# Kernel optimization log

Hardware: AMD Instinct MI355X
Metric: run time of the kernel (lower is better)

## Reference

```python
import jax, jax.numpy as jnp
import numpy as np

NUM_CLUSTERS = 16
CHANNELS = 256
UPDATE_RATE = 0.2
# channels % num_clusters == 0 -> all cluster capacities equal
_BASE = CHANNELS // NUM_CLUSTERS
_REM = CHANNELS % NUM_CLUSTERS
CLUSTER_SIZES = jnp.asarray([_BASE + 1] * _REM + [_BASE] * (NUM_CLUSTERS - _REM), dtype=jnp.int32)


def _cdist(a, b):
    # euclidean pairwise distance, batched over leading dims
    d2 = (jnp.sum(a * a, -1)[..., :, None]
          + jnp.sum(b * b, -1)[..., None, :]
          - 2.0 * (a @ jnp.swapaxes(b, -1, -2)))
    return jnp.sqrt(jnp.clip(d2, 0.0))


def _fps(D, k):
    # farthest point sampling given full [N,N] distance matrix
    start = jnp.argmax(D.sum(1))
    def step(min_d, _):
        far = jnp.argmax(min_d)
        return jnp.minimum(min_d, D[far]), far
    _, rest = jax.lax.scan(step, D[start], None, length=k - 1)
    return jnp.concatenate([start[None], rest])


def _capacity_assign(D, sizes):
    # greedy fixed-capacity assignment, sequential over channels
    order = jnp.argsort(D, axis=1)  # [C, K] cluster preference per channel
    def step(counts, row):
        avail = counts[row] < sizes[row]
        chosen = row[jnp.argmax(avail)]  # first available preference
        return counts.at[chosen].add(1), chosen
    _, assign = jax.lax.scan(step, jnp.zeros(sizes.shape[0], jnp.int32), order)
    return assign


def setup_inputs() -> dict:
    key = jax.random.key(0)
    k1, k2 = jax.random.split(key)
    features = jax.random.normal(k1, (8, CHANNELS, 64, 256), dtype=jnp.float32)
    pos_emb_batch = jax.random.normal(k2, (8, CHANNELS, 3), dtype=jnp.float32)
    return {"features": features, "pos_emb_batch": pos_emb_batch}


def reference(features, pos_emb_batch):
    b, c, nw, df = features.shape
    K = NUM_CLUSTERS
    pos = pos_emb_batch[0]                                   # [C, 3] (module's pos_emb buffer)
    # _initialize_centers: FPS over electrode positions
    centers = pos[_fps(_cdist(pos, pos), K)]                 # [K, 3]
    # _find_farthest_channels (euclidean): FPS over flattened features per batch
    ff = features.reshape(b, c, -1)
    Db = _cdist(ff, ff)                                      # [b, C, C]
    sel = jax.vmap(lambda D: _fps(D, K))(Db)                 # [b, K]
    # _cluster_euclidean_temp: nearest temp center per channel
    center_coords = pos_emb_batch[jnp.arange(b)[:, None], sel]      # [b, K, 3]
    temp_assign = jnp.argmin(_cdist(pos_emb_batch, center_coords), -1)  # [b, C]
    # per-cluster mean of positions over the whole batch
    flat_a = temp_assign.reshape(-1)
    flat_p = pos_emb_batch.reshape(-1, 3)
    sums = jax.ops.segment_sum(flat_p, flat_a, num_segments=K)
    cnts = jax.ops.segment_sum(jnp.ones(flat_a.shape, jnp.float32), flat_a, num_segments=K)
    avg = jnp.where(cnts[:, None] > 0, sums / jnp.maximum(cnts, 1.0)[:, None], 0.0)
    # match old centers to batch-average temp centers and EMA update
    matching = jnp.argmin(_cdist(centers, avg), axis=1)
    centers = (1.0 - UPDATE_RATE) * centers + UPDATE_RATE * avg[matching]
    # capacity-constrained final assignment
    return _capacity_assign(_cdist(pos, centers), CLUSTER_SIZES)
```

## Files before the change

### kernel.cpp

```cpp
#include <hip/hip_runtime.h>
#include <hip/hip_cooperative_groups.h>

namespace cg = cooperative_groups;

#define NB 8
#define NC 256
#define DF 16384
#define KCL 16
#define SPLITS 16
#define KC (DF / SPLITS)
#define BK 32
#define ITERS (KC / BK)
#define NPAIR 3
#define GEMM_BLOCKS (NPAIR * 2 * NB * SPLITS)

typedef _Float16 half8 __attribute__((ext_vector_type(8)));
typedef _Float16 half4_t __attribute__((ext_vector_type(4)));
typedef float floatx4 __attribute__((ext_vector_type(4)));

__device__ const int TItab[NPAIR] = {0,0,1};
__device__ const int TJtab[NPAIR] = {0,1,1};

__device__ __forceinline__ int argmax256w(float v, float* sv, int* si) {
  int t = threadIdx.x;
  float bv = v; int bi = t;
  #pragma unroll
  for (int s = 32; s >= 1; s >>= 1) {
    float ov = __shfl_down(bv, s);
    int   oi = __shfl_down(bi, s);
    if (ov > bv || (ov == bv && oi < bi)) { bv = ov; bi = oi; }
  }
  int w = t >> 6;
  if ((t & 63) == 0) { sv[w] = bv; si[w] = bi; }
  __syncthreads();
  float rbv = sv[0]; int rbi = si[0];
  #pragma unroll
  for (int k = 1; k < 4; ++k) {
    float ov = sv[k]; int oi = si[k];
    if (ov > rbv || (ov == rbv && oi < rbi)) { rbv = ov; rbi = oi; }
  }
  __syncthreads();
  return rbi;
}

__device__ __forceinline__ int argmax512p(float v, float* sv, int* si) {
  int t = threadIdx.x;
  sv[t] = v; si[t] = t;
  __syncthreads();
  #pragma unroll
  for (int s = 256; s >= 1; s >>= 1) {
    if (t < s) {
      float a = sv[t], b = sv[t + s];
      int ia = si[t], ib = si[t + s];
      if (b > a || (b == a && ib < ia)) { sv[t] = b; si[t] = ib; }
    }
    __syncthreads();
  }
  int r = si[0];
  __syncthreads();
  return r;
}

__global__ __launch_bounds__(512, 3) void k_gemm_pre(const float* __restrict__ ff,
                                                     const float* __restrict__ pe,
                                                     float* __restrict__ Pp,
                                                     float* __restrict__ centers0,
                                                     float* __restrict__ rs) {
  __shared__ _Float16 Ah[128][40];
  __shared__ _Float16 Al[128][40];
  __shared__ _Float16 Bh[64][40];
  __shared__ _Float16 Bl[64][40];

  const int bid = blockIdx.x;
  const int tid = threadIdx.x;

  if (bid == GEMM_BLOCKS) {
    float* sm = (float*)&Ah[0][0];
    float* px = sm;        float* py = sm + 256;
    float* pz = sm + 512;  float* pn = sm + 768;
    float* sv = sm + 1024; int*   si = (int*)(sm + 1536);
    int* fpsIdx = (int*)(sm + 2048);
    const int t = tid;
    for (int i = t; i < NB * NC; i += 512) rs[i] = 0.f;
    const bool valid = t < NC;
    float x = 0.f, y = 0.f, z = 0.f, n = 0.f;
    if (valid) {
      x = pe[t * 3 + 0]; y = pe[t * 3 + 1]; z = pe[t * 3 + 2];
      n = x * x + y * y + z * z;
      px[t] = x; py[t] = y; pz[t] = z; pn[t] = n;
    }
    __syncthreads();
    float rsum = -3.4e38f;
    if (valid) {
      rsum = 0.f;
      for (int j = 0; j < NC; ++j) {
        float dot = x * px[j] + y * py[j] + z * pz[j];
        rsum += sqrtf(fmaxf(n + pn[j] - 2.f * dot, 0.f));
      }
    }
    int start = argmax512p(rsum, sv, si);
    if (t == 0) fpsIdx[0] = start;
    float mind = -3.4e38f;
    if (valid) {
      float dot0 = x * px[start] + y * py[start] + z * pz[start];
      mind = sqrtf(fmaxf(n + pn[start] - 2.f * dot0, 0.f));
    }
    for (int it = 1; it < KCL; ++it) {
      int far = argmax512p(mind, sv, si);
      if (t == 0) fpsIdx[it] = far;
      if (valid) {
        float dot = x * px[far] + y * py[far] + z * pz[far];
        mind = fminf(mind, sqrtf(fmaxf(n + pn[far] - 2.f * dot, 0.f)));
      }
    }
    __syncthreads();
    if (t < KCL) {
      int p = fpsIdx[t];
      centers0[t * 3 + 0] = px[p];
      centers0[t * 3 + 1] = py[p];
      centers0[t * 3 + 2] = pz[p];
    }
    return;
  }

  const int x    = bid & 7;
  const int slot = bid >> 3;
  const int tc   = slot % 6;
  const int u    = slot / 6;
  const int gi   = x * 16 + u;
  const int b    = gi & 7;
  const int sp   = gi >> 3;

  const int pair = tc >> 1, ch = tc & 1;
  const int ti = TItab[pair], tj = TJtab[pair];
  const bool diag = (ti == tj);

  const int wave = tid >> 6, lane = tid & 63;
  const int wr = wave >> 1, wc = wave & 1;
  const int lrow = lane & 15, q = lane >> 4;

  const int srA = tid >> 2, scA = (tid & 3) * 8;
  const int srB = tid >> 3, scB = (tid & 7) * 4;
  const float* gA = ff + ((size_t)(b * NC + ti * 128 + srA)) * DF + sp * KC + scA;
  const float* gB = ff + ((size_t)(b * NC + tj * 128 + ch * 64 + srB)) * DF + sp * KC + scB;

  floatx4 a1[2][2], a2[2][2], a3[2][2];
  #pragma unroll
  for (int i = 0; i < 2; ++i)
    #pragma unroll
    for (int j = 0; j < 2; ++j) { a1[i][j] = (floatx4)0.f; a2[i][j] = (floatx4)0.f; a3[i][j] = (floatx4)0.f; }

  float4 ra0 = *(const float4*)(gA), ra1 = *(const float4*)(gA + 4);
  float4 rb = make_float4(0.f, 0.f, 0.f, 0.f);
  if (!diag) rb = *(const float4*)(gB);
  gA += BK; gB += BK;

  for (int it = 0; it < ITERS; ++it) {
    float fa[8] = {ra0.x, ra0.y, ra0.z, ra0.w, ra1.x, ra1.y, ra1.z, ra1.w};
    half8 ah, al;
    #pragma unroll
    for (int e = 0; e < 8; ++e) {
      _Float16 h = (_Float16)fa[e];
      ah[e] = h;
      al[e] = (_Float16)(fa[e] - (float)h);
    }
    half4_t bh4 = (half4_t)(_Float16)0.f, bl4 = (half4_t)(_Float16)0.f;
    if (!diag) {
      float fb[4] = {rb.x, rb.y, rb.z, rb.w};
      #pragma unroll
      for (int e = 0; e < 4; ++e) {
        _Float16 h = (_Float16)fb[e];
        bh4[e] = h;
        bl4[e] = (_Float16)(fb[e] - (float)h);
      }
    }
    __syncthreads();
    *(half8*)&Ah[srA][scA] = ah;
    *(half8*)&Al[srA][scA] = al;
    if (!diag) {
      *(half4_t*)&Bh[srB][scB] = bh4;
      *(half4_t*)&Bl[srB][scB] = bl4;
    }
    __syncthreads();
    if (it + 1 < ITERS) {
      ra0 = *(const float4*)(gA); ra1 = *(const float4*)(gA + 4);
      if (!diag) rb = *(const float4*)(gB);
      gA += BK; gB += BK;
    }
    const _Float16* bhp = diag ? &Ah[ch * 64][0] : &Bh[0][0];
    const _Float16* blp = diag ? &Al[ch * 64][0] : &Bl[0][0];
    half8 af[2], lf[2];
    #pragma unroll
    for (int i = 0; i < 2; ++i) {
      af[i] = *(const half8*)&Ah[wr * 32 + i * 16 + lrow][q * 8];
      lf[i] = *(const half8*)&Al[wr * 32 + i * 16 + lrow][q * 8];
    }
    #pragma unroll
    for (int j = 0; j < 2; ++j) {
      half8 bhf = *(const half8*)(bhp + (wc * 32 + j * 16 + lrow) * 40 + q * 8);
      half8 blf = *(const half8*)(blp + (wc * 32 + j * 16 + lrow) * 40 + q * 8);
      #pragma unroll
      for (int i = 0; i < 2; ++i) {
        a1[i][j] = __builtin_amdgcn_mfma_f32_16x16x32_f16(af[i], bhf, a1[i][j], 0, 0, 0);
        a2[i][j] = __builtin_amdgcn_mfma_f32_16x16x32_f16(af[i], blf, a2[i][j], 0, 0, 0);
        a3[i][j] = __builtin_amdgcn_mfma_f32_16x16x32_f16(lf[i], bhf, a3[i][j], 0, 0, 0);
      }
    }
  }

  float* Pb = Pp + (size_t)(sp * NB + b) * NC * NC;
  #pragma unroll
  for (int i = 0; i < 2; ++i) {
    int grow = ti * 128 + wr * 32 + i * 16 + q * 4;
    #pragma unroll
    for (int j = 0; j < 2; ++j) {
      int gcol = tj * 128 + ch * 64 + wc * 32 + j * 16 + lrow;
      float4 v;
      v.x = a1[i][j][0] + a2[i][j][0] + a3[i][j][0];
      v.y = a1[i][j][1] + a2[i][j][1] + a3[i][j][1];
      v.z = a1[i][j][2] + a2[i][j][2] + a3[i][j][2];
      v.w = a1[i][j][3] + a2[i][j][3] + a3[i][j][3];
      Pb[(size_t)(grow + 0) * NC + gcol] = v.x;
      Pb[(size_t)(grow + 1) * NC + gcol] = v.y;
      Pb[(size_t)(grow + 2) * NC + gcol] = v.z;
      Pb[(size_t)(grow + 3) * NC + gcol] = v.w;
      if (!diag) *(float4*)&Pb[(size_t)gcol * NC + grow] = v;
    }
  }
}

__global__ __launch_bounds__(256) void k_tail(const float* __restrict__ Pp,
                                              float* __restrict__ Db,
                                              float* __restrict__ rs,
                                              const float* __restrict__ pe,
                                              float* __restrict__ ccoord,
                                              const float* __restrict__ centers0,
                                              int* __restrict__ outp) {
  cg::grid_group grid = cg::this_grid();
  const int t = threadIdx.x;

  {
    __shared__ float dg_s[NC];
    const int b = blockIdx.x >> 5, i0 = (blockIdx.x & 31) * 8;
    float s = 0.f;
    #pragma unroll
    for (int sp = 0; sp < SPLITS; ++sp)
      s += Pp[((size_t)(sp * NB + b) * NC + t) * NC + t];
    dg_s[t] = s;
    __syncthreads();
    float colsum = 0.f;
    for (int ii = 0; ii < 8; ++ii) {
      int i = i0 + ii;
      float acc = 0.f;
      #pragma unroll
      for (int sp = 0; sp < SPLITS; ++sp)
        acc += Pp[((size_t)(sp * NB + b) * NC + i) * NC + t];
      float d2 = dg_s[i] + dg_s[t] - 2.f * acc;
      float d = sqrtf(fmaxf(d2, 0.f));
      Db[((size_t)b * NC + i) * NC + t] = d;
      colsum += d;
    }
    atomicAdd(&rs[b * NC + t], colsum);
  }
  grid.sync();

  {
    __shared__ float sv[4]; __shared__ int si[4];
    __shared__ int fpsIdx[KCL];
    if (blockIdx.x < NB) {
      int b = blockIdx.x;
      const float* D = Db + (size_t)b * NC * NC;
      int start = argmax256w(rs[b * NC + t], sv, si);
      if (t == 0) fpsIdx[0] = start;
      float mind = D[start * NC + t];
      for (int it = 1; it < KCL; ++it) {
        int far = argmax256w(mind, sv, si);
        if (t == 0) fpsIdx[it] = far;
        mind = fminf(mind, D[far * NC + t]);
      }
      __syncthreads();
      if (t < KCL) {
        int p = fpsIdx[t];
        ccoord[(b * KCL + t) * 3 + 0] = pe[(b * NC + p) * 3 + 0];
        ccoord[(b * KCL + t) * 3 + 1] = pe[(b * NC + p) * 3 + 1];
        ccoord[(b * KCL + t) * 3 + 2] = pe[(b * NC + p) * 3 + 2];
      }
    }
  }
  grid.sync();

  if (blockIdx.x == 0) {
    __shared__ float cc[NB * KCL * 3];
    __shared__ float cn[NB * KCL];
    __shared__ float sums[KCL][3];
    __shared__ int cnts[KCL];
    __shared__ float avg[KCL][3];
    __shared__ float an[KCL];
    __shared__ float c0[KCL * 3];
    __shared__ float c1x[KCL], c1y[KCL], c1z[KCL], c1n[KCL];
    __shared__ int order[NC][KCL];
    for (int i = t; i < NB * KCL * 3; i += 256) cc[i] = ccoord[i];
    if (t < KCL * 3) c0[t] = centers0[t];
    if (t < KCL) { sums[t][0] = 0.f; sums[t][1] = 0.f; sums[t][2] = 0.f; cnts[t] = 0; }
    __syncthreads();
    if (t < NB * KCL) {
      float x = cc[t * 3], y = cc[t * 3 + 1], z = cc[t * 3 + 2];
      cn[t] = x * x + y * y + z * z;
    }
    __syncthreads();
    for (int b = 0; b < NB; ++b) {
      int p = b * NC + t;
      float x = pe[p * 3], y = pe[p * 3 + 1], z = pe[p * 3 + 2];
      float n = x * x + y * y + z * z;
      float best = 3.4e38f; int bi = 0;
      #pragma unroll
      for (int k = 0; k < KCL; ++k) {
        int c = b * KCL + k;
        float dot = x * cc[c * 3] + y * cc[c * 3 + 1] + z * cc[c * 3 + 2];
        float d2 = fmaxf(n + cn[c] - 2.f * dot, 0.f);
        if (d2 < best) { best = d2; bi = k; }
      }
      atomicAdd(&sums[bi][0], x);
      atomicAdd(&sums[bi][1], y);
      atomicAdd(&sums[bi][2], z);
      atomicAdd(&cnts[bi], 1);
    }
    __syncthreads();
    if (t < KCL) {
      float c = (float)cnts[t];
      float inv = 1.f / fmaxf(c, 1.f);
      float ax = (cnts[t] > 0) ? sums[t][0] * inv : 0.f;
      float ay = (cnts[t] > 0) ? sums[t][1] * inv : 0.f;
      float az = (cnts[t] > 0) ? sums[t][2] * inv : 0.f;
      avg[t][0] = ax; avg[t][1] = ay; avg[t][2] = az;
      an[t] = ax * ax + ay * ay + az * az;
    }
    __syncthreads();
    if (t < KCL) {
      float x = c0[t * 3], y = c0[t * 3 + 1], z = c0[t * 3 + 2];
      float n = x * x + y * y + z * z;
      float best = 3.4e38f; int bi = 0;
      #pragma unroll
      for (int j = 0; j < KCL; ++j) {
        float dot = x * avg[j][0] + y * avg[j][1] + z * avg[j][2];
        float d2 = fmaxf(n + an[j] - 2.f * dot, 0.f);
        if (d2 < best) { best = d2; bi = j; }
      }
      float nx = 0.8f * x + 0.2f * avg[bi][0];
      float ny = 0.8f * y + 0.2f * avg[bi][1];
      float nz = 0.8f * z + 0.2f * avg[bi][2];
      c1x[t] = nx; c1y[t] = ny; c1z[t] = nz;
      c1n[t] = nx * nx + ny * ny + nz * nz;
    }
    __syncthreads();
    {
      float x = pe[t * 3], y = pe[t * 3 + 1], z = pe[t * 3 + 2];
      float n = x * x + y * y + z * z;
      float v[KCL];
      #pragma unroll
      for (int k = 0; k < KCL; ++k) {
        float dot = x * c1x[k] + y * c1y[k] + z * c1z[k];
        v[k] = fmaxf(n + c1n[k] - 2.f * dot, 0.f);
      }
      bool used[KCL];
      #pragma unroll
      for (int k = 0; k < KCL; ++k) used[k] = false;
      for (int r = 0; r < KCL; ++r) {
        float best = 3.4e38f; int bi = 0;
        #pragma unroll
        for (int j = 0; j < KCL; ++j) {
          if (!used[j] && v[j] < best) { best = v[j]; bi = j; }
        }
        order[t][r] = bi;
        used[bi] = true;
      }
    }
    __syncthreads();
    if (t < 64) {
      int cnt = 0;
      int cur = (t < KCL) ? order[0][t] : 0;
      for (int i = 0; i < NC; ++i) {
        int nxt = (t < KCL && i + 1 < NC) ? order[i + 1][t] : 0;
        int ccur = __shfl(cnt, cur);
        bool avail = (t < KCL) && (ccur < 16);
        unsigned long long m = __ballot(avail);
        int chosen;
        if (m != 0ull) {
          int rank = __ffsll((unsigned long long)m) - 1;
          chosen = __shfl(cur, rank);
        } else {
          chosen = __shfl(cur, 0);
        }
        if (t == chosen) cnt++;
        if (t == 0) outp[i] = chosen;
        cur = nxt;
      }
    }
  }
}

extern "C" void kernel_launch(void* const* d_in, const int* in_sizes, int n_in,
                              void* d_out, int out_size, void* d_ws, size_t ws_size,
                              hipStream_t stream) {
  (void)in_sizes; (void)n_in; (void)out_size; (void)ws_size;
  const float* features = (const float*)d_in[0];
  const float* pe = (const float*)d_in[1];
  char* ws = (char*)d_ws;
  float* Pp       = (float*)(ws);
  float* Db       = (float*)(ws + 33554432);
  float* rs       = (float*)(ws + 35651584);
  float* centers0 = (float*)(ws + 35659776);
  float* ccoord   = (float*)(ws + 35660288);
  int*   outp     = (int*)d_out;

  hipLaunchKernelGGL(k_gemm_pre, dim3(GEMM_BLOCKS + 1), dim3(512), 0, stream,
                     features, pe, Pp, centers0, rs);

  void* targs[] = {(void*)&Pp, (void*)&Db, (void*)&rs, (void*)&pe,
                   (void*)&ccoord, (void*)&centers0, (void*)&outp};
  hipLaunchCooperativeKernel((void*)k_tail, dim3(256), dim3(256), targs, 0, stream);
}
```

Baseline: 393.4 us.

## Replace cooperative tail kernel with separate launches and atomic-flag handoff

Splits the cooperative k_tail kernel (two grid.syncs) into k_formD (2048 blocks, one row each) and k_fps_final (8 blocks). The final clustering stage waits on an atomic counter in block 0 instead of a grid barrier. The GEMM now also writes the Gram diagonal into a small dgp buffer, so k_formD no longer gathers strided diagonal entries from the split partials. This removes cooperative-launch and grid-barrier overhead, at the cost of an extra kernel launch, one global atomic per element for the row sums, and a spin-wait that depends on all 8 blocks being resident.

After: 332.2 us. -15.6%, faster.

```diff
diff --git a/kernel.cpp b/kernel.cpp
--- a/kernel.cpp
+++ b/kernel.cpp
@@ -1,7 +1,4 @@
 #include <hip/hip_runtime.h>
-#include <hip/hip_cooperative_groups.h>
-
-namespace cg = cooperative_groups;
 
 #define NB 8
 #define NC 256
@@ -65,7 +62,8 @@
                                                      const float* __restrict__ pe,
                                                      float* __restrict__ Pp,
                                                      float* __restrict__ centers0,
-                                                     float* __restrict__ rs) {
+                                                     float* __restrict__ rs,
+                                                     float* __restrict__ dgp) {
   __shared__ _Float16 Ah[128][40];
   __shared__ _Float16 Al[128][40];
   __shared__ _Float16 Bh[64][40];
@@ -224,177 +222,189 @@
       Pb[(size_t)(grow + 1) * NC + gcol] = v.y;
       Pb[(size_t)(grow + 2) * NC + gcol] = v.z;
       Pb[(size_t)(grow + 3) * NC + gcol] = v.w;
-      if (!diag) *(float4*)&Pb[(size_t)gcol * NC + grow] = v;
-    }
-  }
-}
-
-__global__ __launch_bounds__(256) void k_tail(const float* __restrict__ Pp,
-                                              float* __restrict__ Db,
-                                              float* __restrict__ rs,
-                                              const float* __restrict__ pe,
-                                              float* __restrict__ ccoord,
-                                              const float* __restrict__ centers0,
-                                              int* __restrict__ outp) {
-  cg::grid_group grid = cg::this_grid();
+      if (!diag) {
+        *(float4*)&Pb[(size_t)gcol * NC + grow] = v;
+      } else {
+        int dr = gcol - grow;
+        if (dr >= 0 && dr < 4) {
+          float vr = (dr == 0) ? v.x : (dr == 1) ? v.y : (dr == 2) ? v.z : v.w;
+          dgp[(sp * NB + b) * NC + gcol] = vr;
+        }
+      }
+    }
+  }
+}
+
+__global__ __launch_bounds__(256) void k_formD(const float* __restrict__ Pp,
+                                               const float* __restrict__ dgp,
+                                               float* __restrict__ Db,
+                                               float* __restrict__ rs,
+                                               int* __restrict__ fps_done) {
   const int t = threadIdx.x;
-
+  const int b = blockIdx.x >> 8;
+  const int i = blockIdx.x & 255;
+  if (blockIdx.x == 0 && t == 0) *fps_done = 0;
+  float dgt = 0.f;
+  #pragma unroll
+  for (int sp = 0; sp < SPLITS; ++sp)
+    dgt += dgp[(sp * NB + b) * NC + t];
+  __shared__ float dgi_s;
+  if (t == i) dgi_s = dgt;
+  __syncthreads();
+  float dgi = dgi_s;
+  float acc = 0.f;
+  #pragma unroll
+  for (int sp = 0; sp < SPLITS; ++sp)
+    acc += Pp[((size_t)(sp * NB + b) * NC + i) * NC + t];
+  float d2 = dgi + dgt - 2.f * acc;
+  float d = sqrtf(fmaxf(d2, 0.f));
+  Db[((size_t)b * NC + i) * NC + t] = d;
+  atomicAdd(&rs[b * NC + t], d);
+}
+
+__global__ __launch_bounds__(256) void k_fps_final(const float* __restrict__ Db,
+                                                   const float* __restrict__ rs,
+                                                   const float* __restrict__ pe,
+                                                   const float* __restrict__ centers0,
+                                                   float* __restrict__ ccoord,
+                                                   int* __restrict__ fps_done,
+                                                   int* __restrict__ outp) {
+  const int b = blockIdx.x, t = threadIdx.x;
+  __shared__ float sv[4]; __shared__ int si[4];
+  __shared__ int fpsIdx[KCL];
   {
-    __shared__ float dg_s[NC];
-    const int b = blockIdx.x >> 5, i0 = (blockIdx.x & 31) * 8;
-    float s = 0.f;
-    #pragma unroll
-    for (int sp = 0; sp < SPLITS; ++sp)
-      s += Pp[((size_t)(sp * NB + b) * NC + t) * NC + t];
-    dg_s[t] = s;
-    __syncthreads();
-    float colsum = 0.f;
-    for (int ii = 0; ii < 8; ++ii) {
-      int i = i0 + ii;
-      float acc = 0.f;
-      #pragma unroll
-      for (int sp = 0; sp < SPLITS; ++sp)
-        acc += Pp[((size_t)(sp * NB + b) * NC + i) * NC + t];
-      float d2 = dg_s[i] + dg_s[t] - 2.f * acc;
-      float d = sqrtf(fmaxf(d2, 0.f));
-      Db[((size_t)b * NC + i) * NC + t] = d;
-      colsum += d;
-    }
-    atomicAdd(&rs[b * NC + t], colsum);
-  }
-  grid.sync();
-
+    const float* D = Db + (size_t)b * NC * NC;
+    int start = argmax256w(rs[b * NC + t], sv, si);
+    if (t == 0) fpsIdx[0] = start;
+    float mind = D[start * NC + t];
+    for (int it = 1; it < KCL; ++it) {
+      int far = argmax256w(mind, sv, si);
+      if (t == 0) fpsIdx[it] = far;
+      mind = fminf(mind, D[far * NC + t]);
+    }
+    __syncthreads();
+    if (t < KCL) {
+      int p = fpsIdx[t];
+      ccoord[(b * KCL + t) * 3 + 0] = pe[(b * NC + p) * 3 + 0];
+      ccoord[(b * KCL + t) * 3 + 1] = pe[(b * NC + p) * 3 + 1];
+      ccoord[(b * KCL + t) * 3 + 2] = pe[(b * NC + p) * 3 + 2];
+    }
+  }
+  __syncthreads();
+  if (t == 0)
+    __hip_atomic_fetch_add(fps_done, 1, __ATOMIC_RELEASE, __HIP_MEMORY_SCOPE_AGENT);
+  if (b != 0) return;
+
+  if (t == 0) {
+    while (__hip_atomic_load(fps_done, __ATOMIC_ACQUIRE, __HIP_MEMORY_SCOPE_AGENT) < NB)
+      __builtin_amdgcn_s_sleep(8);
+  }
+  __syncthreads();
+
+  __shared__ float cc[NB * KCL * 3];
+  __shared__ float cn[NB * KCL];
+  __shared__ float sums[KCL][3];
+  __shared__ int cnts[KCL];
+  __shared__ float avg[KCL][3];
+  __shared__ float an[KCL];
+  __shared__ float c0[KCL * 3];
+  __shared__ float c1x[KCL], c1y[KCL], c1z[KCL], c1n[KCL];
+  __shared__ int order[NC][KCL];
+  for (int i = t; i < NB * KCL * 3; i += 256) cc[i] = ccoord[i];
+  if (t < KCL * 3) c0[t] = centers0[t];
+  if (t < KCL) { sums[t][0] = 0.f; sums[t][1] = 0.f; sums[t][2] = 0.f; cnts[t] = 0; }
+  __syncthreads();
+  if (t < NB * KCL) {
+    float x = cc[t * 3], y = cc[t * 3 + 1], z = cc[t * 3 + 2];
+    cn[t] = x * x + y * y + z * z;
+  }
+  __syncthreads();
+  for (int bb = 0; bb < NB; ++bb) {
+    int p = bb * NC + t;
+    float x = pe[p * 3], y = pe[p * 3 + 1], z = pe[p * 3 + 2];
+    float n = x * x + y * y + z * z;
+    float best = 3.4e38f; int bi = 0;
+    #pragma unroll
+    for (int k = 0; k < KCL; ++k) {
+      int c = bb * KCL + k;
+      float dot = x * cc[c * 3] + y * cc[c * 3 + 1] + z * cc[c * 3 + 2];
+      float d2 = fmaxf(n + cn[c] - 2.f * dot, 0.f);
+      if (d2 < best) { best = d2; bi = k; }
+    }
+    atomicAdd(&sums[bi][0], x);
+    atomicAdd(&sums[bi][1], y);
+    atomicAdd(&sums[bi][2], z);
+    atomicAdd(&cnts[bi], 1);
+  }
+  __syncthreads();
+  if (t < KCL) {
+    float c = (float)cnts[t];
+    float inv = 1.f / fmaxf(c, 1.f);
+    float ax = (cnts[t] > 0) ? sums[t][0] * inv : 0.f;
+    float ay = (cnts[t] > 0) ? sums[t][1] * inv : 0.f;
+    float az = (cnts[t] > 0) ? sums[t][2] * inv : 0.f;
+    avg[t][0] = ax; avg[t][1] = ay; avg[t][2] = az;
+    an[t] = ax * ax + ay * ay + az * az;
+  }
+  __syncthreads();
+  if (t < KCL) {
+    float x = c0[t * 3], y = c0[t * 3 + 1], z = c0[t * 3 + 2];
+    float n = x * x + y * y + z * z;
+    float best = 3.4e38f; int bi = 0;
+    #pragma unroll
+    for (int j = 0; j < KCL; ++j) {
+      float dot = x * avg[j][0] + y * avg[j][1] + z * avg[j][2];
+      float d2 = fmaxf(n + an[j] - 2.f * dot, 0.f);
+      if (d2 < best) { best = d2; bi = j; }
+    }
+    float nx = 0.8f * x + 0.2f * avg[bi][0];
+    float ny = 0.8f * y + 0.2f * avg[bi][1];
+    float nz = 0.8f * z + 0.2f * avg[bi][2];
+    c1x[t] = nx; c1y[t] = ny; c1z[t] = nz;
+    c1n[t] = nx * nx + ny * ny + nz * nz;
+  }
+  __syncthreads();
   {
-    __shared__ float sv[4]; __shared__ int si[4];
-    __shared__ int fpsIdx[KCL];
-    if (blockIdx.x < NB) {
-      int b = blockIdx.x;
-      const float* D = Db + (size_t)b * NC * NC;
-      int start = argmax256w(rs[b * NC + t], sv, si);
-      if (t == 0) fpsIdx[0] = start;
-      float mind = D[start * NC + t];
-      for (int it = 1; it < KCL; ++it) {
-        int far = argmax256w(mind, sv, si);
-        if (t == 0) fpsIdx[it] = far;
-        mind = fminf(mind, D[far * NC + t]);
-      }
-      __syncthreads();
-      if (t < KCL) {
-        int p = fpsIdx[t];
-        ccoord[(b * KCL + t) * 3 + 0] = pe[(b * NC + p) * 3 + 0];
-        ccoord[(b * KCL + t) * 3 + 1] = pe[(b * NC + p) * 3 + 1];
-        ccoord[(b * KCL + t) * 3 + 2] = pe[(b * NC + p) * 3 + 2];
-      }
-    }
-  }
-  grid.sync();
-
-  if (blockIdx.x == 0) {
-    __shared__ float cc[NB * KCL * 3];
-    __shared__ float cn[NB * KCL];
-    __shared__ float sums[KCL][3];
-    __shared__ int cnts[KCL];
-    __shared__ float avg[KCL][3];
-    __shared__ float an[KCL];
-    __shared__ float c0[KCL * 3];
-    __shared__ float c1x[KCL], c1y[KCL], c1z[KCL], c1n[KCL];
-    __shared__ int order[NC][KCL];
-    for (int i = t; i < NB * KCL * 3; i += 256) cc[i] = ccoord[i];
-    if (t < KCL * 3) c0[t] = centers0[t];
-    if (t < KCL) { sums[t][0] = 0.f; sums[t][1] = 0.f; sums[t][2] = 0.f; cnts[t] = 0; }
-    __syncthreads();
-    if (t < NB * KCL) {
-      float x = cc[t * 3], y = cc[t * 3 + 1], z = cc[t * 3 + 2];
-      cn[t] = x * x + y * y + z * z;
-    }
-    __syncthreads();
-    for (int b = 0; b < NB; ++b) {
-      int p = b * NC + t;
-      float x = pe[p * 3], y = pe[p * 3 + 1], z = pe[p * 3 + 2];
-      float n = x * x + y * y + z * z;
-      float best = 3.4e38f; int bi = 0;
-      #pragma unroll
-      for (int k = 0; k < KCL; ++k) {
-        int c = b * KCL + k;
-        float dot = x * cc[c * 3] + y * cc[c * 3 + 1] + z * cc[c * 3 + 2];
-        float d2 = fmaxf(n + cn[c] - 2.f * dot, 0.f);
-        if (d2 < best) { best = d2; bi = k; }
-      }
-      atomicAdd(&sums[bi][0], x);
-      atomicAdd(&sums[bi][1], y);
-      atomicAdd(&sums[bi][2], z);
-      atomicAdd(&cnts[bi], 1);
-    }
-    __syncthreads();
-    if (t < KCL) {
-      float c = (float)cnts[t];
-      float inv = 1.f / fmaxf(c, 1.f);
-      float ax = (cnts[t] > 0) ? sums[t][0] * inv : 0.f;
-      float ay = (cnts[t] > 0) ? sums[t][1] * inv : 0.f;
-      float az = (cnts[t] > 0) ? sums[t][2] * inv : 0.f;
-      avg[t][0] = ax; avg[t][1] = ay; avg[t][2] = az;
-      an[t] = ax * ax + ay * ay + az * az;
-    }
-    __syncthreads();
-    if (t < KCL) {
-      float x = c0[t * 3], y = c0[t * 3 + 1], z = c0[t * 3 + 2];
-      float n = x * x + y * y + z * z;
+    float x = pe[t * 3], y = pe[t * 3 + 1], z = pe[t * 3 + 2];
+    float n = x * x + y * y + z * z;
+    float v[KCL];
+    #pragma unroll
+    for (int k = 0; k < KCL; ++k) {
+      float dot = x * c1x[k] + y * c1y[k] + z * c1z[k];
+      v[k] = fmaxf(n + c1n[k] - 2.f * dot, 0.f);
+    }
+    bool used[KCL];
+    #pragma unroll
+    for (int k = 0; k < KCL; ++k) used[k] = false;
+    for (int r = 0; r < KCL; ++r) {
       float best = 3.4e38f; int bi = 0;
       #pragma unroll
       for (int j = 0; j < KCL; ++j) {
-        float dot = x * avg[j][0] + y * avg[j][1] + z * avg[j][2];
-        float d2 = fmaxf(n + an[j] - 2.f * dot, 0.f);
-        if (d2 < best) { best = d2; bi = j; }
-      }
-      float nx = 0.8f * x + 0.2f * avg[bi][0];
-      float ny = 0.8f * y + 0.2f * avg[bi][1];
-      float nz = 0.8f * z + 0.2f * avg[bi][2];
-      c1x[t] = nx; c1y[t] = ny; c1z[t] = nz;
-      c1n[t] = nx * nx + ny * ny + nz * nz;
-    }
-    __syncthreads();
-    {
-      float x = pe[t * 3], y = pe[t * 3 + 1], z = pe[t * 3 + 2];
-      float n = x * x + y * y + z * z;
-      float v[KCL];
-      #pragma unroll
-      for (int k = 0; k < KCL; ++k) {
-        float dot = x * c1x[k] + y * c1y[k] + z * c1z[k];
-        v[k] = fmaxf(n + c1n[k] - 2.f * dot, 0.f);
-      }
-      bool used[KCL];
-      #pragma unroll
-      for (int k = 0; k < KCL; ++k) used[k] = false;
-      for (int r = 0; r < KCL; ++r) {
-        float best = 3.4e38f; int bi = 0;
-        #pragma unroll
-        for (int j = 0; j < KCL; ++j) {
-          if (!used[j] && v[j] < best) { best = v[j]; bi = j; }
-        }
-        order[t][r] = bi;
-        used[bi] = true;
-      }
-    }
-    __syncthreads();
-    if (t < 64) {
-      int cnt = 0;
-      int cur = (t < KCL) ? order[0][t] : 0;
-      for (int i = 0; i < NC; ++i) {
-        int nxt = (t < KCL && i + 1 < NC) ? order[i + 1][t] : 0;
-        int ccur = __shfl(cnt, cur);
-        bool avail = (t < KCL) && (ccur < 16);
-        unsigned long long m = __ballot(avail);
-        int chosen;
-        if (m != 0ull) {
-          int rank = __ffsll((unsigned long long)m) - 1;
-          chosen = __shfl(cur, rank);
-        } else {
-          chosen = __shfl(cur, 0);
-        }
-        if (t == chosen) cnt++;
-        if (t == 0) outp[i] = chosen;
-        cur = nxt;
-      }
+        if (!used[j] && v[j] < best) { best = v[j]; bi = j; }
+      }
+      order[t][r] = bi;
+      used[bi] = true;
+    }
+  }
+  __syncthreads();
+  if (t < 64) {
+    int cnt = 0;
+    int cur = (t < KCL) ? order[0][t] : 0;
+    for (int i = 0; i < NC; ++i) {
+      int nxt = (t < KCL && i + 1 < NC) ? order[i + 1][t] : 0;
+      int ccur = __shfl(cnt, cur);
+      bool avail = (t < KCL) && (ccur < 16);
+      unsigned long long m = __ballot(avail);
+      int chosen;
+      if (m != 0ull) {
+        int rank = __ffsll((unsigned long long)m) - 1;
+        chosen = __shfl(cur, rank);
+      } else {
+        chosen = __shfl(cur, 0);
+      }
+      if (t == chosen) cnt++;
+      if (t == 0) outp[i] = chosen;
+      cur = nxt;
     }
   }
 }
@@ -411,12 +421,14 @@
   float* rs       = (float*)(ws + 35651584);
   float* centers0 = (float*)(ws + 35659776);
   float* ccoord   = (float*)(ws + 35660288);
+  float* dgp      = (float*)(ws + 35661824);
+  int*   fps_done = (int*)  (ws + 35678208);
   int*   outp     = (int*)d_out;
 
   hipLaunchKernelGGL(k_gemm_pre, dim3(GEMM_BLOCKS + 1), dim3(512), 0, stream,
-                     features, pe, Pp, centers0, rs);
-
-  void* targs[] = {(void*)&Pp, (void*)&Db, (void*)&rs, (void*)&pe,
-                   (void*)&ccoord, (void*)&centers0, (void*)&outp};
-  hipLaunchCooperativeKernel((void*)k_tail, dim3(256), dim3(256), targs, 0, stream);
-}
+                     features, pe, Pp, centers0, rs, dgp);
+  hipLaunchKernelGGL(k_formD, dim3(2048), dim3(256), 0, stream,
+                     Pp, dgp, Db, rs, fps_done);
+  hipLaunchKernelGGL(k_fps_final, dim3(NB), dim3(256), 0, stream,
+                     Db, rs, pe, centers0, ccoord, fps_done, outp);
+}
```
